# Kernel optimization log

Measured on AMD Instinct MI355X. Metric: run time of the kernel, lower is better.

The kernel has to match this reference:

```python
import jax, jax.numpy as jnp
import numpy as np

N_S, N_D, E, L = 10000, 2000, 100000, 50000
H = 8            # attention heads
H1, H2, H3 = 128, 128, 64
D_S, D_D = 128, 64
NEG_SLOPE = 0.2  # GATv2 leaky_relu slope


def setup_inputs() -> dict:
    key = jax.random.key(0)
    ks = iter(jax.random.split(key, 48))
    def nrm(shape, fan_in):
        return (jax.random.normal(next(ks), shape) / np.sqrt(fan_in)).astype(jnp.float32)
    inp = {}
    inp["x_snorna"] = jax.random.normal(next(ks), (N_S, D_S), dtype=jnp.float32)
    inp["x_disease"] = jax.random.normal(next(ks), (N_D, D_D), dtype=jnp.float32)
    inp["edge_src"] = jax.random.randint(next(ks), (E,), 0, N_S, dtype=jnp.int32)
    inp["edge_dst"] = jax.random.randint(next(ks), (E,), 0, N_D, dtype=jnp.int32)
    inp["edge_label_src"] = jax.random.randint(next(ks), (L,), 0, N_S, dtype=jnp.int32)
    inp["edge_label_dst"] = jax.random.randint(next(ks), (L,), 0, N_D, dtype=jnp.int32)
    # layer 1: GraphConv per relation (lin_rel has bias, lin_root no bias)
    inp["W1_rel_sd"] = nrm((D_S, H1), D_S); inp["b1_sd"] = jnp.zeros((H1,), jnp.float32)
    inp["W1_root_sd"] = nrm((D_D, H1), D_D)
    inp["W1_rel_ds"] = nrm((D_D, H1), D_D); inp["b1_ds"] = jnp.zeros((H1,), jnp.float32)
    inp["W1_root_ds"] = nrm((D_S, H1), D_S)
    # layer 2: GATv2Conv per relation (lin_l/lin_r with bias, att, final bias)
    for rel in ("sd", "ds"):
        inp[f"Wl2_{rel}"] = nrm((H1, H * H2), H1); inp[f"bl2_{rel}"] = jnp.zeros((H * H2,), jnp.float32)
        inp[f"Wr2_{rel}"] = nrm((H1, H * H2), H1); inp[f"br2_{rel}"] = jnp.zeros((H * H2,), jnp.float32)
        inp[f"att2_{rel}"] = nrm((H, H2), H2)
        inp[f"bias2_{rel}"] = jnp.zeros((H2,), jnp.float32)
    # layer 3: GraphConv per relation
    inp["W3_rel_sd"] = nrm((H2, H3), H2); inp["b3_sd"] = jnp.zeros((H3,), jnp.float32)
    inp["W3_root_sd"] = nrm((H2, H3), H2)
    inp["W3_rel_ds"] = nrm((H2, H3), H2); inp["b3_ds"] = jnp.zeros((H3,), jnp.float32)
    inp["W3_root_ds"] = nrm((H2, H3), H2)
    return inp


def graph_conv(x_src, x_dst, es, ed, W_rel, b_rel, W_root, n_dst):
    # PyG GraphConv: lin_rel(sum-aggregated neighbor feats) + lin_root(x_dst)
    agg = jax.ops.segment_sum(x_src[es], ed, num_segments=n_dst)
    return agg @ W_rel + b_rel + x_dst @ W_root


def gatv2(x_src, x_dst, es, ed, Wl, bl, Wr, br, att, bias, n_dst):
    # PyG GATv2Conv, bipartite, add_self_loops=False, concat=False (mean over heads)
    xl = (x_src @ Wl + bl).reshape(x_src.shape[0], H, -1)  # [Ns,H,C]
    xr = (x_dst @ Wr + br).reshape(x_dst.shape[0], H, -1)  # [Nd,H,C]
    xj = xl[es]                                            # [E,H,C] source msgs
    e = jax.nn.leaky_relu(xj + xr[ed], NEG_SLOPE)          # [E,H,C]
    score = jnp.einsum('ehc,hc->eh', e, att)               # [E,H]
    m = jax.ops.segment_max(score, ed, num_segments=n_dst)
    a = jnp.exp(score - m[ed])
    denom = jax.ops.segment_sum(a, ed, num_segments=n_dst)
    alpha = a / denom[ed]                                  # softmax over in-edges of dst
    out = jax.ops.segment_sum(alpha[:, :, None] * xj, ed, num_segments=n_dst)
    return out.mean(axis=1) + bias                         # concat=False -> head mean


def reference(x_snorna, x_disease, edge_src, edge_dst, edge_label_src, edge_label_dst,
              W1_rel_sd, b1_sd, W1_root_sd, W1_rel_ds, b1_ds, W1_root_ds,
              Wl2_sd, bl2_sd, Wr2_sd, br2_sd, att2_sd, bias2_sd,
              Wl2_ds, bl2_ds, Wr2_ds, br2_ds, att2_ds, bias2_ds,
              W3_rel_sd, b3_sd, W3_root_sd, W3_rel_ds, b3_ds, W3_root_ds):
    # HeteroConv layer 1 (GraphConv both directions); each type has one incoming relation
    xd = graph_conv(x_snorna, x_disease, edge_src, edge_dst, W1_rel_sd, b1_sd, W1_root_sd, N_D)
    xs = graph_conv(x_disease, x_snorna, edge_dst, edge_src, W1_rel_ds, b1_ds, W1_root_ds, N_S)
    xs, xd = jax.nn.relu(xs), jax.nn.relu(xd)  # dropout = identity (eval mode)
    # HeteroConv layer 2 (GATv2Conv both directions)
    xd2 = gatv2(xs, xd, edge_src, edge_dst, Wl2_sd, bl2_sd, Wr2_sd, br2_sd, att2_sd, bias2_sd, N_D)
    xs2 = gatv2(xd, xs, edge_dst, edge_src, Wl2_ds, bl2_ds, Wr2_ds, br2_ds, att2_ds, bias2_ds, N_S)
    xs2, xd2 = jax.nn.relu(xs2), jax.nn.relu(xd2)
    # HeteroConv layer 3 (GraphConv, no activation)
    xd3 = graph_conv(xs2, xd2, edge_src, edge_dst, W3_rel_sd, b3_sd, W3_root_sd, N_D)
    xs3 = graph_conv(xd2, xs2, edge_dst, edge_src, W3_rel_ds, b3_ds, W3_root_ds, N_S)
    # Classifier: per-pair dot product
    return (xs3[edge_label_src] * xd3[edge_label_dst]).sum(axis=-1)
```

## Files before the change

kernel.cpp:

```cpp
#include <hip/hip_runtime.h>
#include <math.h>

#define NEG 0.2f
static const int N_S = 10000, N_D = 2000, E_N = 100000, L_N = 50000;
#define CAP_D 128
#define CAP_S 64

using short8 = __attribute__((ext_vector_type(8))) short;
using f32x4  = __attribute__((ext_vector_type(4))) float;
typedef _Float16 h2 __attribute__((ext_vector_type(2)));

union U8h { uint4 u[2]; h2 h[8]; unsigned w[8]; };

__device__ inline unsigned short f2bf(float f) {
  unsigned u = __float_as_uint(f);
  u += 0x7fff + ((u >> 16) & 1);
  return (unsigned short)(u >> 16);
}
__device__ inline float bf2f(unsigned short u) {
  return __uint_as_float((unsigned)u << 16);
}
__device__ inline unsigned short f2h(float f) {
  _Float16 h = (_Float16)f;
  unsigned short r;
  __builtin_memcpy(&r, &h, 2);
  return r;
}
__device__ inline float h2lo(unsigned u) {
  h2 v; __builtin_memcpy(&v, &u, 4); return (float)v[0];
}
__device__ inline float h2hi(unsigned u) {
  h2 v; __builtin_memcpy(&v, &u, 4); return (float)v[1];
}
__device__ inline h2 u2h2(unsigned u) {
  h2 v; __builtin_memcpy(&v, &u, 4); return v;
}

#define LOG2E 1.4426950408889634f
struct PkD { const float* W; unsigned short* P; int K, M; };
struct Pk12 { PkD d[12]; };
struct PrepArgs {
  const float *xs, *xd;
  unsigned short *xsb, *xdb;
  const float *att_sd, *att_ds;
  unsigned short *att16;
  float *zbias;
};
__global__ void k_prep(PrepArgs a, Pk12 g) {
  int bid = blockIdx.x, t = threadIdx.x;
  if (bid < 1375) {
    int i = bid * 256 + t;
    const int ns4 = N_S * 32;
    if (i < ns4) {
      float4 v = ((const float4*)a.xs)[i];
      ushort4 o = {f2bf(v.x), f2bf(v.y), f2bf(v.z), f2bf(v.w)};
      ((ushort4*)a.xsb)[i] = o;
    } else {
      int j = i - ns4;
      float4 v = ((const float4*)a.xd)[j];
      ushort4 o = {f2bf(v.x), f2bf(v.y), f2bf(v.z), f2bf(v.w)};
      ((ushort4*)a.xdb)[j] = o;
    }
  } else if (bid < 2143) {
    int sub = bid - 1375;
    PkD d = g.d[sub >> 6];
    int total = d.K * d.M, mt = d.M >> 4;
    int lM = 31 - __clz(d.M);
    for (int tid = (sub & 63) * 256 + t; tid < total; tid += 64 * 256) {
      int k = tid >> lM, col = tid & (d.M - 1);
      int kt = k >> 5, kr = k & 31;
      int lg = kr >> 3, r = kr & 7;
      int ct = col >> 4, lo = col & 15;
      d.P[(((kt * mt + ct) * 64) + lg * 16 + lo) * 8 + r] = f2bf(d.W[tid]);
    }
  } else {
    int i = (bid - 2143) * 256 + t;
    if (i < 2048) {
      float v = (i < 1024) ? a.att_sd[i] : a.att_ds[i - 1024];
      a.att16[i] = f2h(v * LOG2E);
    } else if (i < 2112) {
      a.zbias[i - 2048] = 0.f;
    }
  }
}

__global__ void k_bucket(const int* __restrict__ es, const int* __restrict__ ed,
                         int* __restrict__ cnt_d, int* __restrict__ cnt_s,
                         int* __restrict__ bkt_d, int* __restrict__ bkt_s, int E) {
  int e = blockIdx.x * 256 + threadIdx.x;
  if (e >= E) return;
  int s = es[e], d = ed[e];
  int pd = atomicAdd(&cnt_d[d], 1);
  if (pd < CAP_D) bkt_d[d * CAP_D + pd] = s;
  int ps = atomicAdd(&cnt_s[s], 1);
  if (ps < CAP_S) bkt_s[s * CAP_S + ps] = d;
}

__device__ __forceinline__ void gath128(const unsigned short* __restrict__ x,
                                        const int* __restrict__ cnt,
                                        const int* __restrict__ bkt, int CAP,
                                        unsigned short* __restrict__ out,
                                        int n, int half, int cl) {
  int b = n * CAP, e = b + cnt[n];
  float a0 = 0.f, a1 = 0.f, a2 = 0.f, a3 = 0.f;
  int i = b + half;
  for (; i + 2 < e; i += 4) {
    uint2 v0 = *(const uint2*)(x + (long long)bkt[i] * 128 + cl * 4);
    uint2 v1 = *(const uint2*)(x + (long long)bkt[i + 2] * 128 + cl * 4);
    a0 += bf2f((unsigned short)(v0.x & 0xffff)) + bf2f((unsigned short)(v1.x & 0xffff));
    a1 += bf2f((unsigned short)(v0.x >> 16))    + bf2f((unsigned short)(v1.x >> 16));
    a2 += bf2f((unsigned short)(v0.y & 0xffff)) + bf2f((unsigned short)(v1.y & 0xffff));
    a3 += bf2f((unsigned short)(v0.y >> 16))    + bf2f((unsigned short)(v1.y >> 16));
  }
  for (; i < e; i += 2) {
    uint2 v0 = *(const uint2*)(x + (long long)bkt[i] * 128 + cl * 4);
    a0 += bf2f((unsigned short)(v0.x & 0xffff));
    a1 += bf2f((unsigned short)(v0.x >> 16));
    a2 += bf2f((unsigned short)(v0.y & 0xffff));
    a3 += bf2f((unsigned short)(v0.y >> 16));
  }
  a0 += __shfl_xor(a0, 32); a1 += __shfl_xor(a1, 32);
  a2 += __shfl_xor(a2, 32); a3 += __shfl_xor(a3, 32);
  if (!half) {
    ushort4 o = {f2bf(a0), f2bf(a1), f2bf(a2), f2bf(a3)};
    *(ushort4*)&out[(long long)n * 128 + cl * 4] = o;
  }
}

__global__ __launch_bounds__(256) void k_gather1(
    const unsigned short* __restrict__ xsb, const unsigned short* __restrict__ xdb,
    const int* __restrict__ cnt_d, const int* __restrict__ bkt_d,
    const int* __restrict__ cnt_s, const int* __restrict__ bkt_s,
    unsigned short* __restrict__ aggd, unsigned short* __restrict__ aggs) {
  int wv = threadIdx.x >> 6, l = threadIdx.x & 63, half = l >> 5, cl = l & 31;
  int r = blockIdx.x % 6, q = blockIdx.x / 6;
  if (r == 0) {
    gath128(xsb, cnt_d, bkt_d, CAP_D, aggd, q * 4 + wv, half, cl);
  } else {
    int n = (q * 5 + (r - 1)) * 4 + wv;
    if (n >= N_S) return;
    int b = n * CAP_S, e = b + cnt_s[n];
    float a0 = 0.f, a1 = 0.f;
    int i = b + half;
    for (; i + 2 < e; i += 4) {
      unsigned v0 = *(const unsigned*)(xdb + (long long)bkt_s[i] * 64 + cl * 2);
      unsigned v1 = *(const unsigned*)(xdb + (long long)bkt_s[i + 2] * 64 + cl * 2);
      a0 += bf2f((unsigned short)(v0 & 0xffff)) + bf2f((unsigned short)(v1 & 0xffff));
      a1 += bf2f((unsigned short)(v0 >> 16))    + bf2f((unsigned short)(v1 >> 16));
    }
    for (; i < e; i += 2) {
      unsigned v0 = *(const unsigned*)(xdb + (long long)bkt_s[i] * 64 + cl * 2);
      a0 += bf2f((unsigned short)(v0 & 0xffff));
      a1 += bf2f((unsigned short)(v0 >> 16));
    }
    a0 += __shfl_xor(a0, 32); a1 += __shfl_xor(a1, 32);
    if (!half) {
      ushort2 o = {f2bf(a0), f2bf(a1)};
      *(ushort2*)&aggs[(long long)n * 64 + cl * 2] = o;
    }
  }
}

__global__ __launch_bounds__(256) void k_gather3(
    const unsigned short* __restrict__ XPs, const unsigned short* __restrict__ XPd,
    const float* __restrict__ ROOTd, const float* __restrict__ ROOTs,
    const int* __restrict__ cnt_d, const int* __restrict__ bkt_d,
    const int* __restrict__ cnt_s, const int* __restrict__ bkt_s,
    unsigned short* __restrict__ XD3, unsigned short* __restrict__ XS3) {
  int wv = threadIdx.x >> 6, l = threadIdx.x & 63, half = l >> 5, cl = l & 31;
  int r = blockIdx.x % 6, q = blockIdx.x / 6;
  const unsigned short* xp; const float* root; unsigned short* out;
  const int *cnt, *bkt; int n, CAP;
  if (r == 0) {
    n = q * 4 + wv; xp = XPs; root = ROOTd; out = XD3;
    cnt = cnt_d; bkt = bkt_d; CAP = CAP_D;
  } else {
    n = (q * 5 + (r - 1)) * 4 + wv;
    if (n >= N_S) return;
    xp = XPd; root = ROOTs; out = XS3;
    cnt = cnt_s; bkt = bkt_s; CAP = CAP_S;
  }
  int b = n * CAP, e = b + cnt[n];
  float a0 = 0.f, a1 = 0.f;
  int i = b + half;
  for (; i + 2 < e; i += 4) {
    unsigned v0 = *(const unsigned*)(xp + (long long)bkt[i] * 64 + cl * 2);
    unsigned v1 = *(const unsigned*)(xp + (long long)bkt[i + 2] * 64 + cl * 2);
    a0 += h2lo(v0) + h2lo(v1);
    a1 += h2hi(v0) + h2hi(v1);
  }
  for (; i < e; i += 2) {
    unsigned v0 = *(const unsigned*)(xp + (long long)bkt[i] * 64 + cl * 2);
    a0 += h2lo(v0);
    a1 += h2hi(v0);
  }
  a0 += __shfl_xor(a0, 32); a1 += __shfl_xor(a1, 32);
  if (!half) {
    float2 rt = *(const float2*)&root[(long long)n * 64 + cl * 2];
    ushort2 o = {f2h(a0 + rt.x), f2h(a1 + rt.y)};
    *(ushort2*)&out[(long long)n * 64 + cl * 2] = o;
  }
}

struct GD {
  const unsigned short *A0, *P0, *A1, *P1;
  const float* bias;
  void* out;
  int K0, K1, N, M, relu, outmode, y0;
};
template<int ND> struct GDs { GD d[ND]; };

template<int ND>
__global__ __launch_bounds__(256) void k_mfma(GDs<ND> g) {
  __shared__ short ldsB[12288];
  int by = blockIdx.y;
  int di = 0;
  #pragma unroll
  for (int i = 1; i < ND; ++i) if (by >= g.d[i].y0) di = i;
  GD d = g.d[di];
  int ytile = by - d.y0;
  int c0 = blockIdx.x * 64;
  if (c0 >= d.M) return;
  int w = threadIdx.x >> 6, l = threadIdx.x & 63;
  int t = threadIdx.x;
  int r0 = ytile * 64 + w * 16;
  int lg = l >> 4, lo = l & 15;
  int mt = d.M >> 4;
  int ct0 = c0 >> 4;
  int nk0 = d.K0 >> 5, nk1 = d.K1 >> 5;
  for (int kt = 0; kt < nk0; ++kt)
    *(short8*)&ldsB[kt * 2048 + t * 8] =
        *(const short8*)(d.P0 + (long long)(kt * mt + ct0) * 512 + t * 8);
  int ofs1 = nk0 * 2048;
  for (int kt = 0; kt < nk1; ++kt)
    *(short8*)&ldsB[ofs1 + kt * 2048 + t * 8] =
        *(const short8*)(d.P1 + (long long)(kt * mt + ct0) * 512 + t * 8);
  __syncthreads();
  if (r0 >= d.N) return;
  f32x4 acc[4] = {};
  int arow = r0 + lo; arow = (arow < d.N) ? arow : (d.N - 1);
  const unsigned short* a0p = d.A0 + (long long)arow * d.K0 + lg * 8;
  for (int kt = 0; kt < nk0; ++kt) {
    short8 a = *(const short8*)(a0p + kt * 32);
    #pragma unroll
    for (int ct = 0; ct < 4; ++ct) {
      short8 b = *(const short8*)&ldsB[kt * 2048 + (ct * 64 + l) * 8];
      acc[ct] = __builtin_amdgcn_mfma_f32_16x16x32_bf16(a, b, acc[ct], 0, 0, 0);
    }
  }
  if (d.K1) {
    const unsigned short* a1p = d.A1 + (long long)arow * d.K1 + lg * 8;
    for (int kt = 0; kt < nk1; ++kt) {
      short8 a = *(const short8*)(a1p + kt * 32);
      #pragma unroll
      for (int ct = 0; ct < 4; ++ct) {
        short8 b = *(const short8*)&ldsB[ofs1 + kt * 2048 + (ct * 64 + l) * 8];
        acc[ct] = __builtin_amdgcn_mfma_f32_16x16x32_bf16(a, b, acc[ct], 0, 0, 0);
      }
    }
  }
  #pragma unroll
  for (int ct = 0; ct < 4; ++ct) {
    int col = c0 + ct * 16 + lo;
    float bv = d.bias[col];
    #pragma unroll
    for (int r = 0; r < 4; ++r) {
      int grow = r0 + lg * 4 + r;
      if (grow < d.N) {
        float v = acc[ct][r] + bv;
        if (d.relu) v = fmaxf(v, 0.f);
        if (d.outmode == 1)
          ((unsigned short*)d.out)[(long long)grow * d.M + col] = f2bf(v);
        else if (d.outmode == 2)
          ((unsigned short*)d.out)[(long long)grow * d.M + col] = f2h(v);
        else
          ((float*)d.out)[(long long)grow * d.M + col] = v;
      }
    }
  }
}

template<int WPN>
__device__ __forceinline__ void gat_node(
    const unsigned short* __restrict__ xl, const unsigned short* __restrict__ xr,
    int base, int deg, const int* __restrict__ srcid,
    const unsigned short* __restrict__ att16, const float* __restrict__ bias,
    unsigned short* __restrict__ outb, int node, int wsub, int l,
    float (*lm)[8], float (*lss)[8], unsigned (*lacc)[8][64]) {
  int h = l >> 3, sub = l & 7;
  int cbase = h * 128 + sub * 16;
  U8h xr8, at8;
  { const uint4* p = (const uint4*)(xr + (long long)node * 1024 + cbase);
    xr8.u[0] = p[0]; xr8.u[1] = p[1]; }
  { const uint4* p = (const uint4*)(att16 + cbase);
    at8.u[0] = p[0]; at8.u[1] = p[1]; }
  const h2 neg2 = {(_Float16)NEG, (_Float16)NEG};
  float m = -INFINITY, s = 0.f;
  h2 acc2[8] = {};
  int b = base, e = base + deg;

  auto ldrow = [&](int idx, U8h& dst) {
    int ic = idx < e - 1 ? idx : e - 1;
    ic = ic > b ? ic : b;
    const uint4* p = (const uint4*)(xl + (long long)srcid[ic] * 1024 + cbase);
    dst.u[0] = p[0]; dst.u[1] = p[1];
  };

  auto process = [&](U8h& x, bool valid) {
    float sc = 0.f;
    #pragma unroll
    for (int j = 0; j < 8; ++j) {
      h2 t = x.h[j] + xr8.h[j];
      h2 lk = __builtin_elementwise_max(t, t * neg2);
      sc = __builtin_amdgcn_fdot2(lk, at8.h[j], sc, false);
    }
    sc += __shfl_xor(sc, 1); sc += __shfl_xor(sc, 2); sc += __shfl_xor(sc, 4);
    if (valid && sc > m + 4.f) {
      float scl = exp2f(m - sc);
      _Float16 sh = (_Float16)scl;
      h2 s2 = {sh, sh};
      #pragma unroll
      for (int j = 0; j < 8; ++j) acc2[j] *= s2;
      s *= scl; m = sc;
    }
    float a = exp2f(sc - m);
    a = valid ? a : 0.f;
    s += a;
    _Float16 ah = (_Float16)(a * 0.00390625f);
    h2 a2 = {ah, ah};
    #pragma unroll
    for (int j = 0; j < 8; ++j) acc2[j] = __builtin_elementwise_fma(a2, x.h[j], acc2[j]);
  };

  int i = b + wsub;
  int nmine = (deg - wsub + WPN - 1) / WPN;
  if (nmine < 0) nmine = 0;
  int npairs = (nmine + 1) >> 1;
  U8h c, d;
  ldrow(i, c);
  ldrow(i + WPN, d);
  for (int it = 0; it < npairs; ++it) {
    int j = i + 2 * WPN;
    U8h n0, n1;
    ldrow(j, n0);
    ldrow(j + WPN, n1);
    process(c, i < e);
    process(d, i + WPN < e);
    c = n0; d = n1; i = j;
  }

  float val[16];
  if constexpr (WPN == 4) {
    if (sub == 0) { lm[wsub][h] = m; lss[wsub][h] = s; }
    U8h tmp;
    #pragma unroll
    for (int j = 0; j < 8; ++j) tmp.h[j] = acc2[j];
    #pragma unroll
    for (int j = 0; j < 8; ++j) lacc[wsub][j][l] = tmp.w[j];
    __syncthreads();
    if (wsub != 0) return;
    float M2 = fmaxf(fmaxf(lm[0][h], lm[1][h]), fmaxf(lm[2][h], lm[3][h]));
    float S = 0.f;
    #pragma unroll
    for (int j = 0; j < 16; ++j) val[j] = 0.f;
    #pragma unroll
    for (int w2 = 0; w2 < 4; ++w2) {
      float scw = (M2 == -INFINITY) ? 0.f : exp2f(lm[w2][h] - M2);
      S = fmaf(scw, lss[w2][h], S);
      #pragma unroll
      for (int j = 0; j < 8; ++j) {
        unsigned uw = lacc[w2][j][l];
        h2 hv; __builtin_memcpy(&hv, &uw, 4);
        val[2 * j]     = fmaf(scw, (float)hv[0], val[2 * j]);
        val[2 * j + 1] = fmaf(scw, (float)hv[1], val[2 * j + 1]);
      }
    }
    float inv = (S > 0.f) ? 256.f / S : 0.f;
    #pragma unroll
    for (int j = 0; j < 16; ++j) val[j] *= inv;
  } else {
    float inv = (s > 0.f) ? 256.f / s : 0.f;
    #pragma unroll
    for (int j = 0; j < 8; ++j) {
      val[2 * j]     = (float)acc2[j][0] * inv;
      val[2 * j + 1] = (float)acc2[j][1] * inv;
    }
  }
  #pragma unroll
  for (int j = 0; j < 16; ++j) {
    val[j] += __shfl_xor(val[j], 8);
    val[j] += __shfl_xor(val[j], 16);
    val[j] += __shfl_xor(val[j], 32);
  }
  if (l < 8) {
    #pragma unroll
    for (int q = 0; q < 4; ++q) {
      float4 bq = *(const float4*)&bias[sub * 16 + q * 4];
      ushort4 o;
      o.x = f2bf(fmaxf(val[q * 4 + 0] * 0.125f + bq.x, 0.f));
      o.y = f2bf(fmaxf(val[q * 4 + 1] * 0.125f + bq.y, 0.f));
      o.z = f2bf(fmaxf(val[q * 4 + 2] * 0.125f + bq.z, 0.f));
      o.w = f2bf(fmaxf(val[q * 4 + 3] * 0.125f + bq.w, 0.f));
      *(ushort4*)&outb[(long long)node * 128 + sub * 16 + q * 4] = o;
    }
  }
}

__global__ __launch_bounds__(256) void k_gat_both(
    const unsigned short* __restrict__ XLsd, const unsigned short* __restrict__ XRsd,
    const int* __restrict__ cnt_d, const int* __restrict__ bkt_d,
    const unsigned short* __restrict__ att_sd, const float* __restrict__ bias_sd,
    unsigned short* __restrict__ XD2b,
    const unsigned short* __restrict__ XLds, const unsigned short* __restrict__ XRds,
    const int* __restrict__ cnt_s, const int* __restrict__ bkt_s,
    const unsigned short* __restrict__ att_ds, const float* __restrict__ bias_ds,
    unsigned short* __restrict__ XS2b) {
  __shared__ float lm[4][8], lss[4][8];
  __shared__ unsigned lacc[4][8][64];
  int widx = threadIdx.x >> 6, l = threadIdx.x & 63;
  int r = blockIdx.x % 9, q = blockIdx.x / 9;
  if (r < 4) {
    int node = q * 4 + r;
    gat_node<4>(XLsd, XRsd, node * CAP_D, cnt_d[node], bkt_d,
                att_sd, bias_sd, XD2b, node, widx, l, lm, lss, lacc);
  } else {
    int node = (q * 5 + (r - 4)) * 4 + widx;
    if (node < N_S)
      gat_node<1>(XLds, XRds, node * CAP_S, cnt_s[node], bkt_s,
                  att_ds, bias_ds, XS2b, node, 0, l, lm, lss, lacc);
  }
}

__global__ void k_dot64(const unsigned short* __restrict__ xs,
                        const unsigned short* __restrict__ xd,
                        const int* __restrict__ ls, const int* __restrict__ ld,
                        float* __restrict__ out, int L) {
  long long t = (long long)blockIdx.x * blockDim.x + threadIdx.x;
  int wave = (int)(t >> 6), lane = (int)(t & 63);
  int q = lane >> 4, sub = lane & 15;
  int eidx = wave * 4 + q;
  if (eidx >= L) return;
  const uint2* a = (const uint2*)(xs + (long long)ls[eidx] * 64);
  const uint2* b = (const uint2*)(xd + (long long)ld[eidx] * 64);
  uint2 va = a[sub], vb = b[sub];
  float v = __builtin_amdgcn_fdot2(u2h2(va.x), u2h2(vb.x), 0.f, false);
  v = __builtin_amdgcn_fdot2(u2h2(va.y), u2h2(vb.y), v, false);
  v += __shfl_xor(v, 1); v += __shfl_xor(v, 2);
  v += __shfl_xor(v, 4); v += __shfl_xor(v, 8);
  if (sub == 0) out[eidx] = v;
}

extern "C" void kernel_launch(void* const* d_in, const int* in_sizes, int n_in,
                              void* d_out, int out_size, void* d_ws, size_t ws_size,
                              hipStream_t stream) {
  const float* x_s = (const float*)d_in[0];
  const float* x_d = (const float*)d_in[1];
  const int* esrc = (const int*)d_in[2];
  const int* edst = (const int*)d_in[3];
  const int* lsrc = (const int*)d_in[4];
  const int* ldst = (const int*)d_in[5];
  const float* W1rel_sd  = (const float*)d_in[6];
  const float* b1_sd     = (const float*)d_in[7];
  const float* W1root_sd = (const float*)d_in[8];
  const float* W1rel_ds  = (const float*)d_in[9];
  const float* b1_ds     = (const float*)d_in[10];
  const float* W1root_ds = (const float*)d_in[11];
  const float *Wl2_sd = (const float*)d_in[12], *bl2_sd = (const float*)d_in[13],
              *Wr2_sd = (const float*)d_in[14], *br2_sd = (const float*)d_in[15],
              *att2_sd = (const float*)d_in[16], *bias2_sd = (const float*)d_in[17];
  const float *Wl2_ds = (const float*)d_in[18], *bl2_ds = (const float*)d_in[19],
              *Wr2_ds = (const float*)d_in[20], *br2_ds = (const float*)d_in[21],
              *att2_ds = (const float*)d_in[22], *bias2_ds = (const float*)d_in[23];
  const float *W3rel_sd = (const float*)d_in[24], *b3_sd = (const float*)d_in[25],
              *W3root_sd = (const float*)d_in[26];
  const float *W3rel_ds = (const float*)d_in[27], *b3_ds = (const float*)d_in[28],
              *W3root_ds = (const float*)d_in[29];
  float* out = (float*)d_out;

  float* w = (float*)d_ws;
  long long off = 0;
  auto alloc = [&](long long n) { float* p = w + off; off += (n + 63) & ~63LL; return p; };
  unsigned short* xsb   = (unsigned short*)alloc((long long)N_S * 64);
  unsigned short* xdb   = (unsigned short*)alloc((long long)N_D * 32);
  unsigned short* AGGDb = (unsigned short*)alloc((long long)N_D * 64);
  unsigned short* AGGSb = (unsigned short*)alloc((long long)N_S * 32);
  unsigned short* XS1b  = (unsigned short*)alloc((long long)N_S * 64);
  unsigned short* XD1b  = (unsigned short*)alloc((long long)N_D * 64);
  unsigned short* XLsd  = (unsigned short*)alloc((long long)N_S * 512);
  unsigned short* XRsd  = (unsigned short*)alloc((long long)N_D * 512);
  unsigned short* XLds  = (unsigned short*)alloc((long long)N_D * 512);
  unsigned short* XRds  = (unsigned short*)alloc((long long)N_S * 512);
  unsigned short* XS2b  = (unsigned short*)alloc((long long)N_S * 64);
  unsigned short* XD2b  = (unsigned short*)alloc((long long)N_D * 64);
  unsigned short* XPs   = (unsigned short*)alloc((long long)N_S * 32);
  unsigned short* XPd   = (unsigned short*)alloc((long long)N_D * 32);
  float* ROOTd = alloc((long long)N_D * 64);
  float* ROOTs = alloc((long long)N_S * 64);
  unsigned short* XS3h = (unsigned short*)alloc((long long)N_S * 32);
  unsigned short* XD3h = (unsigned short*)alloc((long long)N_D * 32);
  unsigned short* att16 = (unsigned short*)alloc(1024 + 64);
  float* zbias = alloc(64);
  unsigned short* pk[12];
  const int pksz[12] = {128 * 128, 64 * 128, 64 * 128, 128 * 128,
                        131072, 131072, 131072, 131072,
                        128 * 64, 128 * 64, 128 * 64, 128 * 64};
  for (int i = 0; i < 12; ++i) pk[i] = (unsigned short*)alloc(pksz[i] / 2 + 64);
  int* Z = (int*)alloc(2048 + 10048 + (long long)N_D * CAP_D + (long long)N_S * CAP_S + 64);
  int* cnt_d = Z;
  int* cnt_s = Z + 2048;
  int* bkt_d = Z + 2048 + 10048;
  int* bkt_s = bkt_d + N_D * CAP_D;
  const size_t zbytes = (size_t)(2048 + 10048 + N_D * CAP_D + N_S * CAP_S) * 4;
  (void)ws_size; (void)in_sizes; (void)n_in; (void)out_size;

  hipMemsetAsync(Z, 0, zbytes, stream);
  PrepArgs pa = {x_s, x_d, xsb, xdb, att2_sd, att2_ds, att16, zbias};
  Pk12 pkk = {{{W1rel_sd, pk[0], 128, 128}, {W1root_sd, pk[1], 64, 128},
               {W1rel_ds, pk[2], 64, 128},  {W1root_ds, pk[3], 128, 128},
               {Wl2_sd, pk[4], 128, 1024},  {Wr2_sd, pk[5], 128, 1024},
               {Wl2_ds, pk[6], 128, 1024},  {Wr2_ds, pk[7], 128, 1024},
               {W3rel_sd, pk[8], 128, 64},  {W3root_sd, pk[9], 128, 64},
               {W3rel_ds, pk[10], 128, 64}, {W3root_ds, pk[11], 128, 64}}};
  k_prep<<<2152, 256, 0, stream>>>(pa, pkk);
  k_bucket<<<391, 256, 0, stream>>>(esrc, edst, cnt_d, cnt_s, bkt_d, bkt_s, E_N);

  k_gather1<<<3000, 256, 0, stream>>>(xsb, xdb, cnt_d, bkt_d, cnt_s, bkt_s,
                                      AGGDb, AGGSb);
  {
    GDs<2> g = {{{AGGDb, pk[0], xdb, pk[1], b1_sd, XD1b, 128, 64, N_D, 128, 1, 1, 0},
                 {AGGSb, pk[2], xsb, pk[3], b1_ds, XS1b, 64, 128, N_S, 128, 1, 1, 32}}};
    k_mfma<2><<<dim3(2, 189), 256, 0, stream>>>(g);
  }

  {
    GDs<4> g = {{{XS1b, pk[4], nullptr, nullptr, bl2_sd, XLsd, 128, 0, N_S, 1024, 0, 2, 0},
                 {XD1b, pk[5], nullptr, nullptr, br2_sd, XRsd, 128, 0, N_D, 1024, 0, 2, 157},
                 {XD1b, pk[6], nullptr, nullptr, bl2_ds, XLds, 128, 0, N_D, 1024, 0, 2, 189},
                 {XS1b, pk[7], nullptr, nullptr, br2_ds, XRds, 128, 0, N_S, 1024, 0, 2, 221}}};
    k_mfma<4><<<dim3(16, 378), 256, 0, stream>>>(g);
  }
  k_gat_both<<<4500, 256, 0, stream>>>(
      XLsd, XRsd, cnt_d, bkt_d, att16, bias2_sd, XD2b,
      XLds, XRds, cnt_s, bkt_s, att16 + 1024, bias2_ds, XS2b);

  {
    GDs<4> g = {{{XS2b, pk[8],  nullptr, nullptr, zbias, XPs,   128, 0, N_S, 64, 0, 2, 0},
                 {XD2b, pk[10], nullptr, nullptr, zbias, XPd,   128, 0, N_D, 64, 0, 2, 157},
                 {XD2b, pk[9],  nullptr, nullptr, b3_sd, ROOTd, 128, 0, N_D, 64, 0, 0, 189},
                 {XS2b, pk[11], nullptr, nullptr, b3_ds, ROOTs, 128, 0, N_S, 64, 0, 0, 221}}};
    k_mfma<4><<<dim3(1, 378), 256, 0, stream>>>(g);
  }
  k_gather3<<<3000, 256, 0, stream>>>(XPs, XPd, ROOTd, ROOTs,
                                      cnt_d, bkt_d, cnt_s, bkt_s, XD3h, XS3h);

  k_dot64<<<(L_N * 16 + 255) / 256, 256, 0, stream>>>(XS3h, XD3h, lsrc, ldst, out, L_N);
}
```

Baseline: 177.2 us.

## Fuse bucketing into prep, prefetch GAT neighbor ids, widen dot-product loads

Merges the edge bucketing kernel into the prep kernel as extra blocks, removing one launch. In the GATv2 aggregation, neighbor source ids are loaded one iteration ahead so row loads no longer wait on the index load. The fp16 accumulation scaling is folded into the exp2 argument, and the final pair dot product uses 8 lanes with 16-byte loads per pair. Atomic bucketing now runs concurrently with conversion blocks, and the exp offset slightly changes fp16 rounding behavior.

```diff
diff --git a/kernel.cpp b/kernel.cpp
--- a/kernel.cpp
+++ b/kernel.cpp
@@ -40,6 +40,8 @@
 struct PkD { const float* W; unsigned short* P; int K, M; };
 struct Pk12 { PkD d[12]; };
 struct PrepArgs {
+  const int *es, *ed;
+  int *cnt_d, *cnt_s, *bkt_d, *bkt_s;
   const float *xs, *xd;
   unsigned short *xsb, *xdb;
   const float *att_sd, *att_ds;
@@ -48,8 +50,16 @@
 };
 __global__ void k_prep(PrepArgs a, Pk12 g) {
   int bid = blockIdx.x, t = threadIdx.x;
-  if (bid < 1375) {
-    int i = bid * 256 + t;
+  if (bid < 391) {
+    int e = bid * 256 + t;
+    if (e >= E_N) return;
+    int s = a.es[e], d = a.ed[e];
+    int pd = atomicAdd(&a.cnt_d[d], 1);
+    if (pd < CAP_D) a.bkt_d[d * CAP_D + pd] = s;
+    int ps = atomicAdd(&a.cnt_s[s], 1);
+    if (ps < CAP_S) a.bkt_s[s * CAP_S + ps] = d;
+  } else if (bid < 391 + 1375) {
+    int i = (bid - 391) * 256 + t;
     const int ns4 = N_S * 32;
     if (i < ns4) {
       float4 v = ((const float4*)a.xs)[i];
@@ -61,8 +71,8 @@
       ushort4 o = {f2bf(v.x), f2bf(v.y), f2bf(v.z), f2bf(v.w)};
       ((ushort4*)a.xdb)[j] = o;
     }
-  } else if (bid < 2143) {
-    int sub = bid - 1375;
+  } else if (bid < 391 + 1375 + 768) {
+    int sub = bid - 391 - 1375;
     PkD d = g.d[sub >> 6];
     int total = d.K * d.M, mt = d.M >> 4;
     int lM = 31 - __clz(d.M);
@@ -74,7 +84,7 @@
       d.P[(((kt * mt + ct) * 64) + lg * 16 + lo) * 8 + r] = f2bf(d.W[tid]);
     }
   } else {
-    int i = (bid - 2143) * 256 + t;
+    int i = (bid - 391 - 1375 - 768) * 256 + t;
     if (i < 2048) {
       float v = (i < 1024) ? a.att_sd[i] : a.att_ds[i - 1024];
       a.att16[i] = f2h(v * LOG2E);
@@ -82,18 +92,6 @@
       a.zbias[i - 2048] = 0.f;
     }
   }
-}
-
-__global__ void k_bucket(const int* __restrict__ es, const int* __restrict__ ed,
-                         int* __restrict__ cnt_d, int* __restrict__ cnt_s,
-                         int* __restrict__ bkt_d, int* __restrict__ bkt_s, int E) {
-  int e = blockIdx.x * 256 + threadIdx.x;
-  if (e >= E) return;
-  int s = es[e], d = ed[e];
-  int pd = atomicAdd(&cnt_d[d], 1);
-  if (pd < CAP_D) bkt_d[d * CAP_D + pd] = s;
-  int ps = atomicAdd(&cnt_s[s], 1);
-  if (ps < CAP_S) bkt_s[s * CAP_S + ps] = d;
 }
 
 __device__ __forceinline__ void gath128(const unsigned short* __restrict__ x,
@@ -299,10 +297,12 @@
   h2 acc2[8] = {};
   int b = base, e = base + deg;
 
-  auto ldrow = [&](int idx, U8h& dst) {
+  auto cl = [&](int idx) {
     int ic = idx < e - 1 ? idx : e - 1;
-    ic = ic > b ? ic : b;
-    const uint4* p = (const uint4*)(xl + (long long)srcid[ic] * 1024 + cbase);
+    return ic > b ? ic : b;
+  };
+  auto ldid = [&](int sid, U8h& dst) {
+    const uint4* p = (const uint4*)(xl + (long long)sid * 1024 + cbase);
     dst.u[0] = p[0]; dst.u[1] = p[1];
   };
 
@@ -323,10 +323,10 @@
       for (int j = 0; j < 8; ++j) acc2[j] *= s2;
       s *= scl; m = sc;
     }
-    float a = exp2f(sc - m);
+    float a = exp2f(sc - m - 8.f);
     a = valid ? a : 0.f;
     s += a;
-    _Float16 ah = (_Float16)(a * 0.00390625f);
+    _Float16 ah = (_Float16)a;
     h2 a2 = {ah, ah};
     #pragma unroll
     for (int j = 0; j < 8; ++j) acc2[j] = __builtin_elementwise_fma(a2, x.h[j], acc2[j]);
@@ -336,17 +336,20 @@
   int nmine = (deg - wsub + WPN - 1) / WPN;
   if (nmine < 0) nmine = 0;
   int npairs = (nmine + 1) >> 1;
+  int s0 = srcid[cl(i)], s1 = srcid[cl(i + WPN)];
   U8h c, d;
-  ldrow(i, c);
-  ldrow(i + WPN, d);
+  ldid(s0, c);
+  ldid(s1, d);
+  int s2 = srcid[cl(i + 2 * WPN)], s3 = srcid[cl(i + 3 * WPN)];
   for (int it = 0; it < npairs; ++it) {
-    int j = i + 2 * WPN;
     U8h n0, n1;
-    ldrow(j, n0);
-    ldrow(j + WPN, n1);
+    ldid(s2, n0);
+    ldid(s3, n1);
+    int s4 = srcid[cl(i + 4 * WPN)], s5 = srcid[cl(i + 5 * WPN)];
     process(c, i < e);
     process(d, i + WPN < e);
-    c = n0; d = n1; i = j;
+    c = n0; d = n1; s2 = s4; s3 = s5;
+    i += 2 * WPN;
   }
 
   float val[16];
@@ -375,11 +378,11 @@
         val[2 * j + 1] = fmaf(scw, (float)hv[1], val[2 * j + 1]);
       }
     }
-    float inv = (S > 0.f) ? 256.f / S : 0.f;
+    float inv = (S > 0.f) ? 1.f / S : 0.f;
     #pragma unroll
     for (int j = 0; j < 16; ++j) val[j] *= inv;
   } else {
-    float inv = (s > 0.f) ? 256.f / s : 0.f;
+    float inv = (s > 0.f) ? 1.f / s : 0.f;
     #pragma unroll
     for (int j = 0; j < 8; ++j) {
       val[2 * j]     = (float)acc2[j][0] * inv;
@@ -437,16 +440,17 @@
                         float* __restrict__ out, int L) {
   long long t = (long long)blockIdx.x * blockDim.x + threadIdx.x;
   int wave = (int)(t >> 6), lane = (int)(t & 63);
-  int q = lane >> 4, sub = lane & 15;
-  int eidx = wave * 4 + q;
+  int q = lane >> 3, sub = lane & 7;
+  int eidx = wave * 8 + q;
   if (eidx >= L) return;
-  const uint2* a = (const uint2*)(xs + (long long)ls[eidx] * 64);
-  const uint2* b = (const uint2*)(xd + (long long)ld[eidx] * 64);
-  uint2 va = a[sub], vb = b[sub];
+  const uint4* a = (const uint4*)(xs + (long long)ls[eidx] * 64);
+  const uint4* b = (const uint4*)(xd + (long long)ld[eidx] * 64);
+  uint4 va = a[sub], vb = b[sub];
   float v = __builtin_amdgcn_fdot2(u2h2(va.x), u2h2(vb.x), 0.f, false);
   v = __builtin_amdgcn_fdot2(u2h2(va.y), u2h2(vb.y), v, false);
-  v += __shfl_xor(v, 1); v += __shfl_xor(v, 2);
-  v += __shfl_xor(v, 4); v += __shfl_xor(v, 8);
+  v = __builtin_amdgcn_fdot2(u2h2(va.z), u2h2(vb.z), v, false);
+  v = __builtin_amdgcn_fdot2(u2h2(va.w), u2h2(vb.w), v, false);
+  v += __shfl_xor(v, 1); v += __shfl_xor(v, 2); v += __shfl_xor(v, 4);
   if (sub == 0) out[eidx] = v;
 }
 
@@ -514,15 +518,15 @@
   (void)ws_size; (void)in_sizes; (void)n_in; (void)out_size;
 
   hipMemsetAsync(Z, 0, zbytes, stream);
-  PrepArgs pa = {x_s, x_d, xsb, xdb, att2_sd, att2_ds, att16, zbias};
+  PrepArgs pa = {esrc, edst, cnt_d, cnt_s, bkt_d, bkt_s,
+                 x_s, x_d, xsb, xdb, att2_sd, att2_ds, att16, zbias};
   Pk12 pkk = {{{W1rel_sd, pk[0], 128, 128}, {W1root_sd, pk[1], 64, 128},
                {W1rel_ds, pk[2], 64, 128},  {W1root_ds, pk[3], 128, 128},
                {Wl2_sd, pk[4], 128, 1024},  {Wr2_sd, pk[5], 128, 1024},
                {Wl2_ds, pk[6], 128, 1024},  {Wr2_ds, pk[7], 128, 1024},
                {W3rel_sd, pk[8], 128, 64},  {W3root_sd, pk[9], 128, 64},
                {W3rel_ds, pk[10], 128, 64}, {W3root_ds, pk[11], 128, 64}}};
-  k_prep<<<2152, 256, 0, stream>>>(pa, pkk);
-  k_bucket<<<391, 256, 0, stream>>>(esrc, edst, cnt_d, cnt_s, bkt_d, bkt_s, E_N);
+  k_prep<<<2543, 256, 0, stream>>>(pa, pkk);
 
   k_gather1<<<3000, 256, 0, stream>>>(xsb, xdb, cnt_d, bkt_d, cnt_s, bkt_s,
                                       AGGDb, AGGSb);
@@ -553,5 +557,5 @@
   k_gather3<<<3000, 256, 0, stream>>>(XPs, XPd, ROOTd, ROOTs,
                                       cnt_d, bkt_d, cnt_s, bkt_s, XD3h, XS3h);
 
-  k_dot64<<<(L_N * 16 + 255) / 256, 256, 0, stream>>>(XS3h, XD3h, lsrc, ldst, out, L_N);
-}
+  k_dot64<<<(L_N * 8 + 255) / 256, 256, 0, stream>>>(XS3h, XD3h, lsrc, ldst, out, L_N);
+}
```

Measured after the change: 172.3 us. 2.8% less time.
